# Optimization experiments

Measured on AMD Instinct MI355X. Metric: run time of the kernel, lower is better.

Reference implementation:

```python
import jax, jax.numpy as jnp
import numpy as np

N_NODES = 50000
N_EDGES = 1000000
N_GRAPHS = 256
ORIG = 92
ATOM = 64
NBR = 41
EPS = 1e-5


def _bn_train(h, gamma, beta):
    # BatchNorm1d in training mode: batch stats, biased variance
    mu = h.mean(axis=0)
    var = jnp.var(h, axis=0)
    return (h - mu) * jax.lax.rsqrt(var + EPS) * gamma + beta


def setup_inputs() -> dict:
    key = jax.random.key(0)
    ks = jax.random.split(key, 16)
    inp = {
        "x": jax.random.normal(ks[0], (N_NODES, ORIG), dtype=jnp.float32),
        "edge_attr": jax.random.normal(ks[1], (N_EDGES, NBR), dtype=jnp.float32),
        "lower_f": jax.random.normal(ks[2], (N_NODES, ATOM), dtype=jnp.float32),
        "edge_index": jax.random.randint(ks[3], (2, N_EDGES), 0, N_NODES, dtype=jnp.int32),
        "batch": jnp.sort(jax.random.randint(ks[4], (N_NODES,), 0, N_GRAPHS, dtype=jnp.int32)),
        # params
        "emb_W": jax.random.normal(ks[5], (ORIG, ATOM), dtype=jnp.float32) / np.sqrt(ORIG),
        "emb_b": jnp.zeros((ATOM,), dtype=jnp.float32),
        "fc_W": jax.random.normal(ks[6], (2 * ATOM + NBR, 2 * ATOM), dtype=jnp.float32) / np.sqrt(2 * ATOM + NBR),
        "fc_b": jnp.zeros((2 * ATOM,), dtype=jnp.float32),
        "bn1_g": jnp.ones((2 * ATOM,), dtype=jnp.float32),
        "bn1_b": jnp.zeros((2 * ATOM,), dtype=jnp.float32),
        "bn2_g": jnp.ones((ATOM,), dtype=jnp.float32),
        "bn2_b": jnp.zeros((ATOM,), dtype=jnp.float32),
        "att_W": jax.random.normal(ks[7], (ATOM, 1), dtype=jnp.float32) / np.sqrt(ATOM),
        "att_b": jnp.zeros((1,), dtype=jnp.float32),
        "out_W": jax.random.normal(ks[8], (ATOM, 1), dtype=jnp.float32) / np.sqrt(ATOM),
        "out_b": jnp.zeros((1,), dtype=jnp.float32),
    }
    return inp


def reference(x, edge_attr, lower_f, emb_W, emb_b, fc_W, fc_b, bn1_g, bn1_b,
              bn2_g, bn2_b, att_W, att_b, out_W, out_b, edge_index, batch):
    # embedding + lower-level features
    atom_fea = x @ emb_W + emb_b + lower_f  # [N, ATOM]

    # CGConv: gather endpoints, concat with edge features
    src, dst = edge_index[0], edge_index[1]
    total = jnp.concatenate([atom_fea[src], atom_fea[dst], edge_attr], axis=-1)  # [E, 2A+NBR]
    gated = _bn_train(total @ fc_W + fc_b, bn1_g, bn1_b)  # [E, 2A]
    nbr_filter, nbr_core = gated[:, :ATOM], gated[:, ATOM:]
    msg = jax.nn.sigmoid(nbr_filter) * jax.nn.softplus(nbr_core)  # [E, A]
    summed = jax.ops.segment_sum(msg, src, num_segments=N_NODES)  # [N, A]
    atom_out = _bn_train(summed, bn2_g, bn2_b)

    # SiLU + attentional aggregation per graph
    h = jax.nn.silu(atom_out)  # [N, A]
    logits = (h @ att_W + att_b)[:, 0]  # [N]
    seg_max = jax.ops.segment_max(logits, batch, num_segments=N_GRAPHS)
    e = jnp.exp(logits - seg_max[batch])
    denom = jax.ops.segment_sum(e, batch, num_segments=N_GRAPHS)
    alpha = e / denom[batch]  # [N]
    crys = jax.ops.segment_sum(alpha[:, None] * h, batch, num_segments=N_GRAPHS)  # [G, A]
    crys_fea = crys @ out_W + out_b  # [G, 1]
    return atom_out, crys_fea
```

## Files before the change

### kernel.cpp

```cpp
#include <hip/hip_runtime.h>
#include <math.h>

#define NN 50000
#define NE 1000000
#define NG 256
#define ORIGD 92
#define NBRD 41
#define NSPREAD 32
#define SCAN_B 256

typedef unsigned short u16;
typedef __attribute__((ext_vector_type(8))) short short8;
typedef __attribute__((ext_vector_type(4))) float f32x4;
typedef __attribute__((ext_vector_type(8))) float f32x8;

#define OFF_AFB     0
#define OFF_SUMMED  1600000
#define OFF_WT      4800000
#define OFF_BN1SPR  4812288
#define OFF_BN1SC   4820480
#define OFF_BN2ACC  4820736
#define OFF_BN2SC   4820864
#define OFF_ELOG    4820992
#define OFF_SEGMAX  4870992
#define OFF_DENOM   4871248
#define OFF_CNT     4871504
#define OFF_PTR     4921504
#define OFF_HEAD    4971504
#define OFF_BSUM    5021504
#define OFF_BOFS    5021760
#define OFF_EIDX    5022016
#define OFF_H       6022016
#define OFF_T2_END  70022016
#define OFF_P       70022016
#define OFF_T3_END  82822016
#define OFF_SRCC    82822016
#define OFF_DSTC    83822016
#define OFF_EAB     84822016
#define OFF_T4_END  108822016

__device__ __forceinline__ u16 f2b(float f) {
    unsigned u = __float_as_uint(f);
    return (u16)((u + 0x7FFFu + ((u >> 16) & 1u)) >> 16);
}
__device__ __forceinline__ float b2f(u16 u) {
    return __uint_as_float(((unsigned)u) << 16);
}
__device__ __forceinline__ float gate(float f, float cc) {
    float sig = __builtin_amdgcn_rcpf(1.f + __expf(-f));
    float sp  = fmaxf(cc, 0.f) + __logf(1.f + __expf(-fabsf(cc)));
    return sig * sp;
}
__device__ __forceinline__ float fsilu(float x) {
    return x * __builtin_amdgcn_rcpf(1.f + __expf(-x));
}

__global__ __launch_bounds__(256) void k_embed2(
    const float* __restrict__ x, const float* __restrict__ lf,
    const float* __restrict__ W, const float* __restrict__ b,
    u16* __restrict__ afb, const float* __restrict__ fcW,
    u16* __restrict__ wT3, u16* __restrict__ wP, float* __restrict__ ws)
{
    int gid = blockIdx.x * 256 + threadIdx.x;
    int n = gid >> 6, c = gid & 63;
    const float* xr = x + (long)n * ORIGD;
    float acc = b[c] + lf[gid];
#pragma unroll 4
    for (int k = 0; k < ORIGD; k++)
        acc = fmaf(xr[k], W[k * 64 + c], acc);
    afb[gid] = f2b(acc);

    if (blockIdx.x < 96) {
        int i = blockIdx.x * 256 + threadIdx.x;
        if (i < 8192) {
            int j = i >> 6, k = i & 63;
            wT3[i] = (k < NBRD) ? f2b(fcW[(128 + k) * 128 + j]) : (u16)0;
        } else {
            int i2 = i - 8192;
            int j = i2 >> 6, k = i2 & 63;
            int row = (j < 128) ? k : (64 + k);
            wP[i2] = f2b(fcW[row * 128 + (j & 127)]);
        }
    } else if (blockIdx.x < 336) {
        int zid = (blockIdx.x - 96) * 256 + threadIdx.x;
        if (zid < 8704) {
            ws[OFF_BN1SPR + zid] = 0.f;
        } else {
            int z2 = zid - 8704;
            if (z2 < 50512) ws[OFF_SEGMAX + z2] = 0.f;
        }
    }
}

__global__ void k_prepw(const float* __restrict__ fcW, u16* __restrict__ wT)
{
    int i = blockIdx.x * 256 + threadIdx.x;
    int j = i / 192, k = i - j * 192;
    wT[i] = (k < 169) ? f2b(fcW[k * 128 + j]) : (u16)0;
}

__global__ void k_prepw2(const float* __restrict__ fcW, u16* __restrict__ wT3,
                         u16* __restrict__ wP)
{
    int i = blockIdx.x * 256 + threadIdx.x;
    if (i < 8192) {
        int j = i >> 6, k = i & 63;
        wT3[i] = (k < NBRD) ? f2b(fcW[(128 + k) * 128 + j]) : (u16)0;
    } else {
        int i2 = i - 8192;
        int j = i2 >> 6, k = i2 & 63;
        int row = (j < 128) ? k : (64 + k);
        wP[i2] = f2b(fcW[row * 128 + (j & 127)]);
    }
}

__global__ __launch_bounds__(256) void k_embed(
    const float* __restrict__ x, const float* __restrict__ lf,
    const float* __restrict__ W, const float* __restrict__ b,
    u16* __restrict__ afb)
{
    int gid = blockIdx.x * 256 + threadIdx.x;
    int n = gid >> 6, c = gid & 63;
    const float* xr = x + (long)n * ORIGD;
    float acc = b[c] + lf[gid];
#pragma unroll 4
    for (int k = 0; k < ORIGD; k++)
        acc = fmaf(xr[k], W[k * 64 + c], acc);
    afb[gid] = f2b(acc);
}

template <int PACKED>
__global__ __launch_bounds__(256) void k_pnode(
    const u16* __restrict__ afb, const u16* __restrict__ wP, float* __restrict__ P)
{
    __shared__ __align__(16) u16 sB[64 * 72];
    const int tid = threadIdx.x;
    const int n0 = blockIdx.x * 64;

    for (int i = tid; i < 512; i += 256) {
        int r = i >> 3, c = i & 7;
        int n = n0 + r;
        short8 v = {0,0,0,0,0,0,0,0};
        if (n < NN) v = *(const short8*)(afb + (long)n * 64 + c * 8);
        *(short8*)(sB + r * 72 + c * 8) = v;
    }
    __syncthreads();

    const int lane = tid & 63, w = tid >> 6;
    const int n16 = lane & 15, quad = lane >> 4;
    short8 A[4][2];
#pragma unroll
    for (int m = 0; m < 4; m++) {
        const u16* base = wP + (16 * (w + 4 * m) + n16) * 64 + quad * 8;
        A[m][0] = *(const short8*)(base);
        A[m][1] = *(const short8*)(base + 32);
    }
    for (int t = 0; t < 4; t++) {
        const u16* row = sB + (16 * t + n16) * 72 + quad * 8;
        short8 b0 = *(const short8*)(row);
        short8 b1 = *(const short8*)(row + 32);
        int n = n0 + 16 * t + n16;
#pragma unroll
        for (int m = 0; m < 4; m++) {
            f32x4 acc = {0.f, 0.f, 0.f, 0.f};
            acc = __builtin_amdgcn_mfma_f32_16x16x32_bf16(A[m][0], b0, acc, 0, 0, 0);
            acc = __builtin_amdgcn_mfma_f32_16x16x32_bf16(A[m][1], b1, acc, 0, 0, 0);
            if (n < NN) {
                int M = w + 4 * m;
                int j;
                if (PACKED) {
                    int MM = M & 7;
                    j = ((M >> 3) * 128) + ((MM & 3) * 4 + quad) * 8 + ((MM >> 2) << 2);
                } else {
                    j = 16 * M + 4 * quad;
                }
                *(f32x4*)(P + (long)n * 256 + j) = acc;
            }
        }
    }
}

__global__ void k_hist(const int* __restrict__ ei, int* __restrict__ cnt)
{
    int e = blockIdx.x * 256 + threadIdx.x;
    if (e < NE) atomicAdd(&cnt[ei[e]], 1);
}

__global__ __launch_bounds__(1024) void k_scan1b(const int* __restrict__ cnt,
                                                 int* __restrict__ ptr,
                                                 int* __restrict__ head)
{
    __shared__ int sw[16];
    const int t = threadIdx.x;
    const int CH = (NN + 1023) / 1024;
    const int base = t * CH;
    int s = 0;
    for (int i = 0; i < CH; i++) {
        int n = base + i;
        s += (n < NN) ? cnt[n] : 0;
    }
    int lane = t & 63, wv = t >> 6;
    int v = s;
    for (int o = 1; o < 64; o <<= 1) {
        int x = __shfl_up(v, o, 64);
        if (lane >= o) v += x;
    }
    if (lane == 63) sw[wv] = v;
    __syncthreads();
    if (t == 0) {
        int acc = 0;
        for (int i = 0; i < 16; i++) { int x = sw[i]; sw[i] = acc; acc += x; }
    }
    __syncthreads();
    int p = sw[wv] + (v - s);
    for (int i = 0; i < CH; i++) {
        int n = base + i;
        if (n < NN) { ptr[n] = p; head[n] = p; p += cnt[n]; }
    }
}

__global__ void k_partial(const int* __restrict__ cnt, int* __restrict__ lofs,
                          int* __restrict__ bsum)
{
    __shared__ int sd[SCAN_B];
    int t = threadIdx.x, b = blockIdx.x, n = b * SCAN_B + t;
    int v = (n < NN) ? cnt[n] : 0;
    sd[t] = v; __syncthreads();
    for (int o = 1; o < SCAN_B; o <<= 1) {
        int x = (t >= o) ? sd[t - o] : 0;
        __syncthreads();
        sd[t] += x;
        __syncthreads();
    }
    if (n < NN) lofs[n] = sd[t] - v;
    if (t == SCAN_B - 1) bsum[b] = sd[t];
}

__global__ void k_scanb(const int* __restrict__ bsum, int* __restrict__ bofs, int nb)
{
    __shared__ int sd[256];
    int t = threadIdx.x;
    int v = (t < nb) ? bsum[t] : 0;
    sd[t] = v; __syncthreads();
    for (int o = 1; o < 256; o <<= 1) {
        int x = (t >= o) ? sd[t - o] : 0;
        __syncthreads();
        sd[t] += x;
        __syncthreads();
    }
    bofs[t] = sd[t] - v;
}

__global__ void k_addofs(int* __restrict__ ptr, const int* __restrict__ bofs,
                         int* __restrict__ head)
{
    int n = blockIdx.x * 256 + threadIdx.x;
    if (n < NN) {
        int p = ptr[n] + bofs[n >> 8];
        ptr[n] = p; head[n] = p;
    }
}

__global__ void k_fill(const int* __restrict__ ei, int* __restrict__ head,
                       int* __restrict__ eidx)
{
    int e = blockIdx.x * 256 + threadIdx.x;
    if (e < NE) {
        int pos = atomicAdd(&head[ei[e]], 1);
        eidx[pos] = e;
    }
}

__global__ __launch_bounds__(256) void k_fill3(
    const int* __restrict__ ei, const float* __restrict__ ea,
    int* __restrict__ head, int* __restrict__ srcC, int* __restrict__ dstC,
    u16* __restrict__ eaB)
{
    int e = blockIdx.x * 256 + threadIdx.x;
    if (e >= NE) return;
    int s = ei[e];
    int pos = atomicAdd(&head[s], 1);
    srcC[pos] = s;
    dstC[pos] = ei[NE + e];
    const float* row = ea + (long)e * NBRD;
    u16* orow = eaB + (long)pos * 48;
#pragma unroll
    for (int q = 0; q < 6; q++) {
        short8 v;
#pragma unroll
        for (int j = 0; j < 8; j++) {
            int c = q * 8 + j;
            v[j] = (c < NBRD) ? (short)f2b(row[c]) : (short)0;
        }
        *(short8*)(orow + q * 8) = v;
    }
}

__global__ __launch_bounds__(256) void k_gemm_h4(
    const u16* __restrict__ eaB, const int* __restrict__ srcC,
    const int* __restrict__ dstC, const u16* __restrict__ wT3,
    const float* __restrict__ P, u16* __restrict__ h,
    float* __restrict__ spread)
{
    const int tid = threadIdx.x;
    const int e0 = blockIdx.x * 64;
    const int lane = tid & 63, w = tid >> 6;
    const int n16 = lane & 15, quad = lane >> 4;

    short8 A0[2], A1[2];
    {
        const u16* a0 = wT3 + (16 * w + n16) * 64 + quad * 8;
        const u16* a1 = wT3 + (16 * (w + 4) + n16) * 64 + quad * 8;
        A0[0] = *(const short8*)(a0);  A0[1] = *(const short8*)(a0 + 32);
        A1[0] = *(const short8*)(a1);  A1[1] = *(const short8*)(a1 + 32);
    }

    const int j0 = 16 * w + 4 * quad;
    const int pofs = (w * 4 + quad) * 8;
    const short8 bz = {0,0,0,0,0,0,0,0};
    float s0[4] = {0,0,0,0}, q0[4] = {0,0,0,0}, s1[4] = {0,0,0,0}, q1[4] = {0,0,0,0};

#pragma unroll
    for (int t = 0; t < 4; t++) {
        const int pos = e0 + 16 * t + n16;
        const int src = srcC[pos];
        const int dst = dstC[pos];

        const u16* er = eaB + (long)pos * 48;
        short8 b0 = *(const short8*)(er + quad * 8);
        short8 b1 = bz;
        if (quad < 2) b1 = *(const short8*)(er + 32 + quad * 8);

        f32x8 gS = *(const f32x8*)(P + (long)src * 256 + pofs);
        f32x8 gD = *(const f32x8*)(P + (long)dst * 256 + 128 + pofs);

        f32x4 acc0 = {0.f, 0.f, 0.f, 0.f}, acc1 = {0.f, 0.f, 0.f, 0.f};
        acc0 = __builtin_amdgcn_mfma_f32_16x16x32_bf16(A0[0], b0, acc0, 0, 0, 0);
        acc0 = __builtin_amdgcn_mfma_f32_16x16x32_bf16(A0[1], b1, acc0, 0, 0, 0);
        acc1 = __builtin_amdgcn_mfma_f32_16x16x32_bf16(A1[0], b0, acc1, 0, 0, 0);
        acc1 = __builtin_amdgcn_mfma_f32_16x16x32_bf16(A1[1], b1, acc1, 0, 0, 0);

        u16 hv0[4], hv1[4];
#pragma unroll
        for (int r = 0; r < 4; r++) {
            float u0 = acc0[r] + gS[r] + gD[r];
            float u1 = acc1[r] + gS[4 + r] + gD[4 + r];
            s0[r] += u0; q0[r] = fmaf(u0, u0, q0[r]);
            s1[r] += u1; q1[r] = fmaf(u1, u1, q1[r]);
            hv0[r] = f2b(u0); hv1[r] = f2b(u1);
        }
        u16* hp = h + (long)pos * 128 + j0;
        ushort4 v0 = make_ushort4(hv0[0], hv0[1], hv0[2], hv0[3]);
        ushort4 v1 = make_ushort4(hv1[0], hv1[1], hv1[2], hv1[3]);
        *(ushort4*)hp = v0;
        *(ushort4*)(hp + 64) = v1;
    }

#pragma unroll
    for (int m = 1; m < 16; m <<= 1) {
#pragma unroll
        for (int r = 0; r < 4; r++) {
            s0[r] += __shfl_xor(s0[r], m); q0[r] += __shfl_xor(q0[r], m);
            s1[r] += __shfl_xor(s1[r], m); q1[r] += __shfl_xor(q1[r], m);
        }
    }
    if (n16 == 0) {
        float* sp = spread + (blockIdx.x & (NSPREAD - 1)) * 256;
#pragma unroll
        for (int r = 0; r < 4; r++) {
            atomicAdd(sp + j0 + r,       s0[r]);
            atomicAdd(sp + 128 + j0 + r, q0[r]);
            atomicAdd(sp + 64 + j0 + r,  s1[r]);
            atomicAdd(sp + 192 + j0 + r, q1[r]);
        }
    }
}

__global__ __launch_bounds__(256) void k_gemm_h2(
    const float* __restrict__ ea, const int* __restrict__ ei,
    const u16* __restrict__ wT3, const float* __restrict__ P,
    u16* __restrict__ h, float* __restrict__ spread)
{
    __shared__ __align__(16) u16 sTl[64 * 72];
    __shared__ int sSrc[64], sDst[64];
    const int tid = threadIdx.x;
    const int e0 = blockIdx.x * 64;

    if (tid < 64) sSrc[tid] = ei[e0 + tid];
    else if (tid < 128) sDst[tid - 64] = ei[NE + e0 + tid - 64];

    for (int i = tid; i < 64 * 64; i += 256) {
        int e = i >> 6, c = i & 63;
        float v = (c < NBRD) ? ea[(long)(e0 + e) * NBRD + c] : 0.f;
        sTl[e * 72 + c] = f2b(v);
    }
    __syncthreads();

    const int lane = tid & 63, w = tid >> 6;
    const int n16 = lane & 15, quad = lane >> 4;

    short8 A0[2], A1[2];
    {
        const u16* b0 = wT3 + (16 * w + n16) * 64 + quad * 8;
        const u16* b1 = wT3 + (16 * (w + 4) + n16) * 64 + quad * 8;
        A0[0] = *(const short8*)(b0);  A0[1] = *(const short8*)(b0 + 32);
        A1[0] = *(const short8*)(b1);  A1[1] = *(const short8*)(b1 + 32);
    }

    const int j0 = 16 * w + 4 * quad;
    float s0[4] = {0,0,0,0}, q0[4] = {0,0,0,0}, s1[4] = {0,0,0,0}, q1[4] = {0,0,0,0};

    for (int t = 0; t < 4; t++) {
        const int ge16 = 16 * t + n16;
        const int src = sSrc[ge16], dst = sDst[ge16];
        const float* pS = P + (long)src * 256;
        const float* pD = P + (long)dst * 256 + 128;
        f32x4 g0 = *(const f32x4*)(pS + j0);
        f32x4 g1 = *(const f32x4*)(pS + 64 + j0);
        f32x4 g2 = *(const f32x4*)(pD + j0);
        f32x4 g3 = *(const f32x4*)(pD + 64 + j0);

        const u16* row = sTl + ge16 * 72 + quad * 8;
        short8 b0 = *(const short8*)(row);
        short8 b1 = *(const short8*)(row + 32);
        f32x4 acc0 = {0.f, 0.f, 0.f, 0.f}, acc1 = {0.f, 0.f, 0.f, 0.f};
        acc0 = __builtin_amdgcn_mfma_f32_16x16x32_bf16(A0[0], b0, acc0, 0, 0, 0);
        acc0 = __builtin_amdgcn_mfma_f32_16x16x32_bf16(A0[1], b1, acc0, 0, 0, 0);
        acc1 = __builtin_amdgcn_mfma_f32_16x16x32_bf16(A1[0], b0, acc1, 0, 0, 0);
        acc1 = __builtin_amdgcn_mfma_f32_16x16x32_bf16(A1[1], b1, acc1, 0, 0, 0);

        u16 hv0[4], hv1[4];
#pragma unroll
        for (int r = 0; r < 4; r++) {
            float u0 = acc0[r] + g0[r] + g2[r];
            float u1 = acc1[r] + g1[r] + g3[r];
            s0[r] += u0; q0[r] = fmaf(u0, u0, q0[r]);
            s1[r] += u1; q1[r] = fmaf(u1, u1, q1[r]);
            hv0[r] = f2b(u0); hv1[r] = f2b(u1);
        }
        int ge = e0 + ge16;
        u16* hp = h + (long)ge * 128 + j0;
        ushort4 v0 = make_ushort4(hv0[0], hv0[1], hv0[2], hv0[3]);
        ushort4 v1 = make_ushort4(hv1[0], hv1[1], hv1[2], hv1[3]);
        *(ushort4*)hp = v0;
        *(ushort4*)(hp + 64) = v1;
    }

#pragma unroll
    for (int m = 1; m < 16; m <<= 1) {
#pragma unroll
        for (int r = 0; r < 4; r++) {
            s0[r] += __shfl_xor(s0[r], m); q0[r] += __shfl_xor(q0[r], m);
            s1[r] += __shfl_xor(s1[r], m); q1[r] += __shfl_xor(q1[r], m);
        }
    }
    if (n16 == 0) {
        float* sp = spread + (blockIdx.x & (NSPREAD - 1)) * 256;
#pragma unroll
        for (int r = 0; r < 4; r++) {
            atomicAdd(sp + j0 + r,       s0[r]);
            atomicAdd(sp + 128 + j0 + r, q0[r]);
            atomicAdd(sp + 64 + j0 + r,  s1[r]);
            atomicAdd(sp + 192 + j0 + r, q1[r]);
        }
    }
}

__global__ __launch_bounds__(256) void k_gemm_h(
    const u16* __restrict__ afb, const float* __restrict__ ea,
    const int* __restrict__ ei, const u16* __restrict__ wT,
    u16* __restrict__ h, float* __restrict__ spread)
{
    __shared__ __align__(16) u16 sTl[64 * 200];
    __shared__ int sSrc[64], sDst[64];
    const int tid = threadIdx.x;
    const int e0 = blockIdx.x * 64;

    if (tid < 64) sSrc[tid] = ei[e0 + tid];
    else if (tid < 128) sDst[tid - 64] = ei[NE + e0 + tid - 64];
    __syncthreads();

    for (int i = tid; i < 1024; i += 256) {
        int e = i >> 4, q = i & 15;
        const u16* g = (q < 8) ? (afb + (long)sSrc[e] * 64 + q * 8)
                               : (afb + (long)sDst[e] * 64 + (q - 8) * 8);
        *(short8*)(sTl + e * 200 + q * 8) = *(const short8*)g;
    }
    for (int i = tid; i < 64 * 64; i += 256) {
        int e = i >> 6, c = i & 63;
        float v = (c < NBRD) ? ea[(long)(e0 + e) * NBRD + c] : 0.f;
        sTl[e * 200 + 128 + c] = f2b(v);
    }
    __syncthreads();

    const int lane = tid & 63, w = tid >> 6;
    const int n16 = lane & 15, quad = lane >> 4;

    short8 A0[6], A1[6];
    {
        const u16* b0 = wT + (16 * w + n16) * 192 + quad * 8;
        const u16* b1 = wT + (16 * (w + 4) + n16) * 192 + quad * 8;
#pragma unroll
        for (int ks = 0; ks < 6; ks++) {
            A0[ks] = *(const short8*)(b0 + ks * 32);
            A1[ks] = *(const short8*)(b1 + ks * 32);
        }
    }

    const int j0 = 16 * w + 4 * quad;
    float s0[4] = {0,0,0,0}, q0[4] = {0,0,0,0}, s1[4] = {0,0,0,0}, q1[4] = {0,0,0,0};

    for (int t = 0; t < 4; t++) {
        const u16* row = sTl + (16 * t + n16) * 200 + quad * 8;
        f32x4 acc0 = {0.f, 0.f, 0.f, 0.f}, acc1 = {0.f, 0.f, 0.f, 0.f};
#pragma unroll
        for (int ks = 0; ks < 6; ks++) {
            short8 b = *(const short8*)(row + ks * 32);
            acc0 = __builtin_amdgcn_mfma_f32_16x16x32_bf16(A0[ks], b, acc0, 0, 0, 0);
            acc1 = __builtin_amdgcn_mfma_f32_16x16x32_bf16(A1[ks], b, acc1, 0, 0, 0);
        }
#pragma unroll
        for (int r = 0; r < 4; r++) {
            s0[r] += acc0[r]; q0[r] = fmaf(acc0[r], acc0[r], q0[r]);
            s1[r] += acc1[r]; q1[r] = fmaf(acc1[r], acc1[r], q1[r]);
        }
        int ge = e0 + 16 * t + n16;
        u16* hp = h + (long)ge * 128 + j0;
        ushort4 v0 = make_ushort4(f2b(acc0[0]), f2b(acc0[1]), f2b(acc0[2]), f2b(acc0[3]));
        ushort4 v1 = make_ushort4(f2b(acc1[0]), f2b(acc1[1]), f2b(acc1[2]), f2b(acc1[3]));
        *(ushort4*)hp = v0;
        *(ushort4*)(hp + 64) = v1;
    }

#pragma unroll
    for (int m = 1; m < 16; m <<= 1) {
#pragma unroll
        for (int r = 0; r < 4; r++) {
            s0[r] += __shfl_xor(s0[r], m); q0[r] += __shfl_xor(q0[r], m);
            s1[r] += __shfl_xor(s1[r], m); q1[r] += __shfl_xor(q1[r], m);
        }
    }
    if (n16 == 0) {
        float* sp = spread + (blockIdx.x & (NSPREAD - 1)) * 256;
#pragma unroll
        for (int r = 0; r < 4; r++) {
            atomicAdd(sp + j0 + r,       s0[r]);
            atomicAdd(sp + 128 + j0 + r, q0[r]);
            atomicAdd(sp + 64 + j0 + r,  s1[r]);
            atomicAdd(sp + 192 + j0 + r, q1[r]);
        }
    }
}

template <int MODE>
__global__ __launch_bounds__(256) void k_gemm(
    const u16* __restrict__ afb, const float* __restrict__ ea,
    const int* __restrict__ ei, const u16* __restrict__ wT,
    const float* __restrict__ sc, float* __restrict__ outbuf)
{
    __shared__ __align__(16) u16 sTl[64 * 200];
    __shared__ int sSrc[64], sDst[64];
    const int tid = threadIdx.x;
    const int e0 = blockIdx.x * 64;

    if (tid < 64) sSrc[tid] = ei[e0 + tid];
    else if (tid < 128) sDst[tid - 64] = ei[NE + e0 + tid - 64];
    __syncthreads();
    for (int i = tid; i < 1024; i += 256) {
        int e = i >> 4, q = i & 15;
        const u16* g = (q < 8) ? (afb + (long)sSrc[e] * 64 + q * 8)
                               : (afb + (long)sDst[e] * 64 + (q - 8) * 8);
        *(short8*)(sTl + e * 200 + q * 8) = *(const short8*)g;
    }
    for (int i = tid; i < 64 * 64; i += 256) {
        int e = i >> 6, c = i & 63;
        float v = (c < NBRD) ? ea[(long)(e0 + e) * NBRD + c] : 0.f;
        sTl[e * 200 + 128 + c] = f2b(v);
    }
    __syncthreads();

    const int lane = tid & 63, w = tid >> 6;
    const int n16 = lane & 15, quad = lane >> 4;
    short8 A0[6], A1[6];
    {
        const u16* b0 = wT + (16 * w + n16) * 192 + quad * 8;
        const u16* b1 = wT + (16 * (w + 4) + n16) * 192 + quad * 8;
#pragma unroll
        for (int ks = 0; ks < 6; ks++) {
            A0[ks] = *(const short8*)(b0 + ks * 32);
            A1[ks] = *(const short8*)(b1 + ks * 32);
        }
    }
    const int j0 = 16 * w + 4 * quad;
    float s0[4] = {0,0,0,0}, q0[4] = {0,0,0,0}, s1[4] = {0,0,0,0}, q1[4] = {0,0,0,0};
    float scf[4], shf[4], scc[4], shc[4];
    if (MODE == 1) {
#pragma unroll
        for (int r = 0; r < 4; r++) {
            scf[r] = sc[j0 + r];        shf[r] = sc[128 + j0 + r];
            scc[r] = sc[64 + j0 + r];   shc[r] = sc[192 + j0 + r];
        }
    }
    for (int t = 0; t < 4; t++) {
        const u16* row = sTl + (16 * t + n16) * 200 + quad * 8;
        f32x4 acc0 = {0.f, 0.f, 0.f, 0.f}, acc1 = {0.f, 0.f, 0.f, 0.f};
#pragma unroll
        for (int ks = 0; ks < 6; ks++) {
            short8 b = *(const short8*)(row + ks * 32);
            acc0 = __builtin_amdgcn_mfma_f32_16x16x32_bf16(A0[ks], b, acc0, 0, 0, 0);
            acc1 = __builtin_amdgcn_mfma_f32_16x16x32_bf16(A1[ks], b, acc1, 0, 0, 0);
        }
        if (MODE == 0) {
#pragma unroll
            for (int r = 0; r < 4; r++) {
                s0[r] += acc0[r]; q0[r] = fmaf(acc0[r], acc0[r], q0[r]);
                s1[r] += acc1[r]; q1[r] = fmaf(acc1[r], acc1[r], q1[r]);
            }
        } else {
            int src = sSrc[16 * t + n16];
            float* dst = outbuf + (long)src * 64 + j0;
#pragma unroll
            for (int r = 0; r < 4; r++) {
                float f  = fmaf(acc0[r], scf[r], shf[r]);
                float cc = fmaf(acc1[r], scc[r], shc[r]);
                atomicAdd(dst + r, gate(f, cc));
            }
        }
    }
    if (MODE == 0) {
#pragma unroll
        for (int m = 1; m < 16; m <<= 1) {
#pragma unroll
            for (int r = 0; r < 4; r++) {
                s0[r] += __shfl_xor(s0[r], m); q0[r] += __shfl_xor(q0[r], m);
                s1[r] += __shfl_xor(s1[r], m); q1[r] += __shfl_xor(q1[r], m);
            }
        }
        if (n16 == 0) {
            float* sp = outbuf + (blockIdx.x & (NSPREAD - 1)) * 256;
#pragma unroll
            for (int r = 0; r < 4; r++) {
                atomicAdd(sp + j0 + r,       s0[r]);
                atomicAdd(sp + 128 + j0 + r, q0[r]);
                atomicAdd(sp + 64 + j0 + r,  s1[r]);
                atomicAdd(sp + 192 + j0 + r, q1[r]);
            }
        }
    }
}

__global__ void k_bn1fin(const float* __restrict__ spread,
                         const float* __restrict__ g, const float* __restrict__ b,
                         float* __restrict__ sc)
{
    int c = threadIdx.x;
    float s = 0.f, q = 0.f;
    for (int k = 0; k < NSPREAD; k++) { s += spread[k * 256 + c]; q += spread[k * 256 + 128 + c]; }
    float mean_acc = s / (float)NE;
    float var = q / (float)NE - mean_acc * mean_acc;
    float scale = g[c] * rsqrtf(var + 1e-5f);
    sc[c] = scale;
    sc[128 + c] = b[c] - mean_acc * scale;
}

__global__ __launch_bounds__(256) void k_scatter3(
    const u16* __restrict__ h, const int* __restrict__ ptr,
    const int* __restrict__ cnt, const float* __restrict__ spread,
    const float* __restrict__ g, const float* __restrict__ b,
    float* __restrict__ summed)
{
    __shared__ float ssc[256];
    int tid = threadIdx.x;
    if (tid < 128) {
        int c = tid;
        float s = 0.f, q = 0.f;
        for (int k = 0; k < NSPREAD; k++) {
            s += spread[k * 256 + c]; q += spread[k * 256 + 128 + c];
        }
        float mean_acc = s / (float)NE;
        float var = q / (float)NE - mean_acc * mean_acc;
        float scale = g[c] * rsqrtf(var + 1e-5f);
        ssc[c] = scale;
        ssc[128 + c] = b[c] - mean_acc * scale;
    }
    __syncthreads();

    int n = blockIdx.x * 4 + (tid >> 6);
    int l = tid & 63;
    int es = l & 7, cg = l >> 3;

    float scf[8], shf[8], scc[8], shc[8];
#pragma unroll
    for (int j = 0; j < 8; j++) {
        scf[j] = ssc[cg * 8 + j];
        shf[j] = ssc[128 + cg * 8 + j];
        scc[j] = ssc[64 + cg * 8 + j];
        shc[j] = ssc[192 + cg * 8 + j];
    }

    int p0 = ptr[n], deg = cnt[n];
    float acc[8] = {0,0,0,0,0,0,0,0};
    for (int i = 0; i < deg; i += 8) {
        int idx = i + es;
        bool valid = idx < deg;
        int row = p0 + (valid ? idx : 0);
        const u16* hr = h + (long)row * 128;
        short8 f8 = *(const short8*)(hr + cg * 8);
        short8 c8 = *(const short8*)(hr + 64 + cg * 8);
#pragma unroll
        for (int j = 0; j < 8; j++) {
            float f  = fmaf(b2f((u16)f8[j]), scf[j], shf[j]);
            float cc = fmaf(b2f((u16)c8[j]), scc[j], shc[j]);
            float gg = gate(f, cc);
            acc[j] += valid ? gg : 0.f;
        }
    }
#pragma unroll
    for (int m = 1; m < 8; m <<= 1)
#pragma unroll
        for (int j = 0; j < 8; j++) acc[j] += __shfl_xor(acc[j], m);
    if (es == 0) {
        float* sp = summed + (long)n * 64 + cg * 8;
        float4 v0 = {acc[0], acc[1], acc[2], acc[3]};
        float4 v1 = {acc[4], acc[5], acc[6], acc[7]};
        *(float4*)sp = v0;
        *(float4*)(sp + 4) = v1;
    }
}

__global__ __launch_bounds__(256) void k_scatter(
    const u16* __restrict__ h, const int* __restrict__ ptr,
    const int* __restrict__ cnt, const int* __restrict__ eidx,
    const float* __restrict__ sc, float* __restrict__ summed)
{
    int tid = threadIdx.x;
    int n = blockIdx.x * 4 + (tid >> 6);
    int l = tid & 63;
    int es = l & 7, cg = l >> 3;

    float4 a0 = *(const float4*)(sc + cg * 8);
    float4 a1 = *(const float4*)(sc + cg * 8 + 4);
    float4 b0 = *(const float4*)(sc + 128 + cg * 8);
    float4 b1 = *(const float4*)(sc + 128 + cg * 8 + 4);
    float4 c0 = *(const float4*)(sc + 64 + cg * 8);
    float4 c1 = *(const float4*)(sc + 64 + cg * 8 + 4);
    float4 d0 = *(const float4*)(sc + 192 + cg * 8);
    float4 d1 = *(const float4*)(sc + 192 + cg * 8 + 4);
    float scf[8] = {a0.x,a0.y,a0.z,a0.w,a1.x,a1.y,a1.z,a1.w};
    float shf[8] = {b0.x,b0.y,b0.z,b0.w,b1.x,b1.y,b1.z,b1.w};
    float scc[8] = {c0.x,c0.y,c0.z,c0.w,c1.x,c1.y,c1.z,c1.w};
    float shc[8] = {d0.x,d0.y,d0.z,d0.w,d1.x,d1.y,d1.z,d1.w};

    int p0 = ptr[n], deg = cnt[n];
    float acc[8] = {0,0,0,0,0,0,0,0};
    for (int i = 0; i < deg; i += 8) {
        int idx = i + es;
        bool valid = idx < deg;
        int e = eidx[p0 + (valid ? idx : 0)];
        const u16* hr = h + (long)e * 128;
        short8 f8 = *(const short8*)(hr + cg * 8);
        short8 c8 = *(const short8*)(hr + 64 + cg * 8);
#pragma unroll
        for (int j = 0; j < 8; j++) {
            float f  = fmaf(b2f((u16)f8[j]), scf[j], shf[j]);
            float cc = fmaf(b2f((u16)c8[j]), scc[j], shc[j]);
            float gg = gate(f, cc);
            acc[j] += valid ? gg : 0.f;
        }
    }
#pragma unroll
    for (int m = 1; m < 8; m <<= 1)
#pragma unroll
        for (int j = 0; j < 8; j++) acc[j] += __shfl_xor(acc[j], m);
    if (es == 0) {
        float* sp = summed + (long)n * 64 + cg * 8;
        float4 v0 = {acc[0], acc[1], acc[2], acc[3]};
        float4 v1 = {acc[4], acc[5], acc[6], acc[7]};
        *(float4*)sp = v0;
        *(float4*)(sp + 4) = v1;
    }
}

__global__ __launch_bounds__(256) void k_bn2stats(const float* __restrict__ summed,
                                                  float* __restrict__ acc2)
{
    int tid = threadIdx.x; int c = tid & 63; int sub = tid >> 6;
    float s = 0.f, q = 0.f;
    for (int r = blockIdx.x * 4 + sub; r < NN; r += 4 * 128) {
        float v = summed[(long)r * 64 + c]; s += v; q = fmaf(v, v, q);
    }
    __shared__ float rs[256], rq[256];
    rs[tid] = s; rq[tid] = q; __syncthreads();
    if (tid < 64) {
        s = rs[tid] + rs[tid + 64] + rs[tid + 128] + rs[tid + 192];
        q = rq[tid] + rq[tid + 64] + rq[tid + 128] + rq[tid + 192];
        atomicAdd(&acc2[tid], s);
        atomicAdd(&acc2[64 + tid], q);
    }
}

__global__ void k_bn2fin(const float* __restrict__ acc2,
                         const float* __restrict__ g, const float* __restrict__ b,
                         float* __restrict__ sc2, const float* __restrict__ outb,
                         float* __restrict__ out)
{
    int c = threadIdx.x;
    if (c < 64) {
        float mean = acc2[c] / (float)NN;
        float var = acc2[64 + c] / (float)NN - mean * mean;
        float scale = g[c] * rsqrtf(var + 1e-5f);
        sc2[c] = scale;
        sc2[64 + c] = b[c] - mean * scale;
    }
    out[(long)NN * 64 + c] = outb[0];
}

__global__ __launch_bounds__(256) void k_nodepost2(
    const float* __restrict__ summed, const float* __restrict__ acc2,
    const float* __restrict__ g, const float* __restrict__ b,
    const float* __restrict__ attW, const float* __restrict__ attb,
    const int* __restrict__ batch, float* __restrict__ out,
    float* __restrict__ elog, unsigned* __restrict__ segmax)
{
    __shared__ float ssc2[128];
    int tid = threadIdx.x;
    if (tid < 64) {
        float mean = acc2[tid] / (float)NN;
        float var = acc2[64 + tid] / (float)NN - mean * mean;
        float scale = g[tid] * rsqrtf(var + 1e-5f);
        ssc2[tid] = scale;
        ssc2[64 + tid] = b[tid] - mean * scale;
    }
    __syncthreads();

    int n = blockIdx.x * 4 + (tid >> 6); int c = tid & 63;
    float v = summed[(long)n * 64 + c];
    float ao = fmaf(v, ssc2[c], ssc2[64 + c]);
    out[(long)n * 64 + c] = ao;
    float h = fsilu(ao);
    float p = h * attW[c];
#pragma unroll
    for (int off = 32; off; off >>= 1) p += __shfl_down(p, off, 64);
    if (c == 0) {
        float logit = p + attb[0];
        elog[n] = logit;
        unsigned u = __float_as_uint(logit);
        u = (u & 0x80000000u) ? ~u : (u | 0x80000000u);
        atomicMax(&segmax[batch[n]], u);
    }
}

__global__ __launch_bounds__(256) void k_nodepost(
    const float* __restrict__ summed, const float* __restrict__ sc2,
    const float* __restrict__ attW, const float* __restrict__ attb,
    const int* __restrict__ batch, float* __restrict__ out,
    float* __restrict__ elog, unsigned* __restrict__ segmax)
{
    int tid = threadIdx.x; int n = blockIdx.x * 4 + (tid >> 6); int c = tid & 63;
    float v = summed[(long)n * 64 + c];
    float ao = fmaf(v, sc2[c], sc2[64 + c]);
    out[(long)n * 64 + c] = ao;
    float h = fsilu(ao);
    float p = h * attW[c];
#pragma unroll
    for (int off = 32; off; off >>= 1) p += __shfl_down(p, off, 64);
    if (c == 0) {
        float logit = p + attb[0];
        elog[n] = logit;
        unsigned u = __float_as_uint(logit);
        u = (u & 0x80000000u) ? ~u : (u | 0x80000000u);
        atomicMax(&segmax[batch[n]], u);
    }
}

__global__ void k_denom2(const int* __restrict__ batch,
                         const unsigned* __restrict__ segmax,
                         float* __restrict__ elog, float* __restrict__ denom,
                         const float* __restrict__ outb, float* __restrict__ out)
{
    int n = blockIdx.x * 256 + threadIdx.x;
    if (n < NG) out[(long)NN * 64 + n] = outb[0];
    if (n >= NN) return;
    int b = batch[n];
    unsigned u = segmax[b];
    u = (u & 0x80000000u) ? (u & 0x7FFFFFFFu) : ~u;
    float e = __expf(elog[n] - __uint_as_float(u));
    elog[n] = e;
    atomicAdd(&denom[b], e);
}

__global__ void k_denom(const int* __restrict__ batch,
                        const unsigned* __restrict__ segmax,
                        float* __restrict__ elog, float* __restrict__ denom)
{
    int n = blockIdx.x * 256 + threadIdx.x;
    if (n >= NN) return;
    int b = batch[n];
    unsigned u = segmax[b];
    u = (u & 0x80000000u) ? (u & 0x7FFFFFFFu) : ~u;
    float e = __expf(elog[n] - __uint_as_float(u));
    elog[n] = e;
    atomicAdd(&denom[b], e);
}

__global__ __launch_bounds__(256) void k_crys(
    const float* __restrict__ atom_out, const float* __restrict__ elog,
    const float* __restrict__ denom, const int* __restrict__ batch,
    const float* __restrict__ outW, float* __restrict__ out)
{
    int tid = threadIdx.x; int n = blockIdx.x * 4 + (tid >> 6); int l = tid & 63;
    int b = batch[n];
    float alpha = elog[n] / denom[b];
    float ao = atom_out[(long)n * 64 + l];
    float p = fsilu(ao) * outW[l];
#pragma unroll
    for (int off = 32; off; off >>= 1) p += __shfl_down(p, off, 64);
    if (l == 0) atomicAdd(&out[(long)NN * 64 + b], alpha * p);
}

extern "C" void kernel_launch(void* const* d_in, const int* in_sizes, int n_in,
                              void* d_out, int out_size, void* d_ws, size_t ws_size,
                              hipStream_t stream)
{
    const float* x    = (const float*)d_in[0];
    const float* eatt = (const float*)d_in[1];
    const float* lf   = (const float*)d_in[2];
    const int*   ei   = (const int*)d_in[3];
    const int*   batch= (const int*)d_in[4];
    const float* embW = (const float*)d_in[5];
    const float* embB = (const float*)d_in[6];
    const float* fcW  = (const float*)d_in[7];
    const float* bn1g = (const float*)d_in[9];
    const float* bn1b = (const float*)d_in[10];
    const float* bn2g = (const float*)d_in[11];
    const float* bn2b = (const float*)d_in[12];
    const float* attW = (const float*)d_in[13];
    const float* attB = (const float*)d_in[14];
    const float* outW = (const float*)d_in[15];
    const float* outB = (const float*)d_in[16];
    float* out = (float*)d_out;
    float* ws  = (float*)d_ws;

    u16* afb  = (u16*)(ws + OFF_AFB);
    u16* wT   = (u16*)(ws + OFF_WT);
    int* cnt  = (int*)(ws + OFF_CNT);
    int* ptr  = (int*)(ws + OFF_PTR);
    int* head = (int*)(ws + OFF_HEAD);
    int* bsum = (int*)(ws + OFF_BSUM);
    int* bofs = (int*)(ws + OFF_BOFS);
    int* eidx = (int*)(ws + OFF_EIDX);
    u16* h    = (u16*)(ws + OFF_H);

    const bool t4 = ws_size >= (size_t)OFF_T4_END * sizeof(float);
    const bool t3 = ws_size >= (size_t)OFF_T3_END * sizeof(float);
    const bool t2 = ws_size >= (size_t)OFF_T2_END * sizeof(float);

    if (t4) {
        u16* wT3  = wT;
        u16* wP   = wT + 8192;
        float* P  = ws + OFF_P;
        int* srcC = (int*)(ws + OFF_SRCC);
        int* dstC = (int*)(ws + OFF_DSTC);
        u16* eaB  = (u16*)(ws + OFF_EAB);
        k_embed2<<<12500, 256, 0, stream>>>(x, lf, embW, embB, afb, fcW, wT3, wP, ws);
        k_hist<<<(NE + 255) / 256, 256, 0, stream>>>(ei, cnt);
        k_scan1b<<<1, 1024, 0, stream>>>(cnt, ptr, head);
        k_fill3<<<(NE + 255) / 256, 256, 0, stream>>>(ei, eatt, head, srcC, dstC, eaB);
        k_pnode<1><<<(NN + 63) / 64, 256, 0, stream>>>(afb, wP, P);
        k_gemm_h4<<<NE / 64, 256, 0, stream>>>(eaB, srcC, dstC, wT3, P, h,
                                               ws + OFF_BN1SPR);
        k_scatter3<<<NN / 4, 256, 0, stream>>>(h, ptr, cnt, ws + OFF_BN1SPR,
                                               bn1g, bn1b, ws + OFF_SUMMED);
        k_bn2stats<<<128, 256, 0, stream>>>(ws + OFF_SUMMED, ws + OFF_BN2ACC);
        k_nodepost2<<<12500, 256, 0, stream>>>(ws + OFF_SUMMED, ws + OFF_BN2ACC,
                                               bn2g, bn2b, attW, attB, batch, out,
                                               ws + OFF_ELOG,
                                               (unsigned*)(ws + OFF_SEGMAX));
        k_denom2<<<196, 256, 0, stream>>>(batch, (const unsigned*)(ws + OFF_SEGMAX),
                                          ws + OFF_ELOG, ws + OFF_DENOM, outB, out);
        k_crys<<<12500, 256, 0, stream>>>(out, ws + OFF_ELOG, ws + OFF_DENOM, batch,
                                          outW, out);
        return;
    }

    k_embed<<<12500, 256, 0, stream>>>(x, lf, embW, embB, afb);

    if (t3) {
        u16* wT3 = wT;
        u16* wP  = wT + 8192;
        float* P = ws + OFF_P;
        k_prepw2<<<96, 256, 0, stream>>>(fcW, wT3, wP);
        hipMemsetAsync(ws + OFF_BN1SPR, 0,
                       (size_t)(OFF_PTR - OFF_BN1SPR) * sizeof(float), stream);
        k_hist<<<(NE + 255) / 256, 256, 0, stream>>>(ei, cnt);
        k_partial<<<(NN + SCAN_B - 1) / SCAN_B, SCAN_B, 0, stream>>>(cnt, ptr, bsum);
        k_scanb<<<1, 256, 0, stream>>>(bsum, bofs, (NN + SCAN_B - 1) / SCAN_B);
        k_addofs<<<(NN + 255) / 256, 256, 0, stream>>>(ptr, bofs, head);
        k_fill<<<(NE + 255) / 256, 256, 0, stream>>>(ei, head, eidx);
        k_pnode<0><<<(NN + 63) / 64, 256, 0, stream>>>(afb, wP, P);
        k_gemm_h2<<<NE / 64, 256, 0, stream>>>(eatt, ei, wT3, P, h, ws + OFF_BN1SPR);
        k_bn1fin<<<1, 128, 0, stream>>>(ws + OFF_BN1SPR, bn1g, bn1b, ws + OFF_BN1SC);
        k_scatter<<<NN / 4, 256, 0, stream>>>(h, ptr, cnt, eidx, ws + OFF_BN1SC,
                                              ws + OFF_SUMMED);
    } else if (t2) {
        k_prepw<<<96, 256, 0, stream>>>(fcW, wT);
        hipMemsetAsync(ws + OFF_BN1SPR, 0,
                       (size_t)(OFF_PTR - OFF_BN1SPR) * sizeof(float), stream);
        k_hist<<<(NE + 255) / 256, 256, 0, stream>>>(ei, cnt);
        k_partial<<<(NN + SCAN_B - 1) / SCAN_B, SCAN_B, 0, stream>>>(cnt, ptr, bsum);
        k_scanb<<<1, 256, 0, stream>>>(bsum, bofs, (NN + SCAN_B - 1) / SCAN_B);
        k_addofs<<<(NN + 255) / 256, 256, 0, stream>>>(ptr, bofs, head);
        k_fill<<<(NE + 255) / 256, 256, 0, stream>>>(ei, head, eidx);
        k_gemm_h<<<NE / 64, 256, 0, stream>>>(afb, eatt, ei, wT, h, ws + OFF_BN1SPR);
        k_bn1fin<<<1, 128, 0, stream>>>(ws + OFF_BN1SPR, bn1g, bn1b, ws + OFF_BN1SC);
        k_scatter<<<NN / 4, 256, 0, stream>>>(h, ptr, cnt, eidx, ws + OFF_BN1SC,
                                              ws + OFF_SUMMED);
    } else {
        k_prepw<<<96, 256, 0, stream>>>(fcW, wT);
        hipMemsetAsync(ws + OFF_SUMMED, 0,
                       (size_t)(OFF_PTR - OFF_SUMMED) * sizeof(float), stream);
        k_gemm<0><<<NE / 64, 256, 0, stream>>>(afb, eatt, ei, wT, ws + OFF_BN1SC,
                                               ws + OFF_BN1SPR);
        k_bn1fin<<<1, 128, 0, stream>>>(ws + OFF_BN1SPR, bn1g, bn1b, ws + OFF_BN1SC);
        k_gemm<1><<<NE / 64, 256, 0, stream>>>(afb, eatt, ei, wT, ws + OFF_BN1SC,
                                               ws + OFF_SUMMED);
    }

    k_bn2stats<<<128, 256, 0, stream>>>(ws + OFF_SUMMED, ws + OFF_BN2ACC);
    k_bn2fin<<<1, 256, 0, stream>>>(ws + OFF_BN2ACC, bn2g, bn2b, ws + OFF_BN2SC,
                                    outB, out);
    k_nodepost<<<12500, 256, 0, stream>>>(ws + OFF_SUMMED, ws + OFF_BN2SC, attW, attB,
                                          batch, out, ws + OFF_ELOG,
                                          (unsigned*)(ws + OFF_SEGMAX));
    k_denom<<<196, 256, 0, stream>>>(batch, (const unsigned*)(ws + OFF_SEGMAX),
                                     ws + OFF_ELOG, ws + OFF_DENOM);
    k_crys<<<12500, 256, 0, stream>>>(out, ws + OFF_ELOG, ws + OFF_DENOM, batch,
                                      outW, out);
}
```

Baseline: 1.280 ms.

## Convert edge_attr in original order, use multi-block scan, prefetch edge loads in GEMM

Edge-attribute bf16 conversion moves out of the atomic fill into the histogram kernel, which converts each edge row coalesced in original order with six threads per edge. The fill kernel now writes only the permutation and the src/dst arrays, and the GEMM gathers edge rows through the permutation index. The single-block 1024-thread scan is replaced by the existing three-kernel multi-block scan. The GEMM software-pipelines its gathers with double buffering and sets occupancy launch bounds, trading a random read of edge rows in the GEMM for coalesced conversion writes.

After: 1.194 ms. 6.7% less time.

```diff
diff --git a/kernel.cpp b/kernel.cpp
--- a/kernel.cpp
+++ b/kernel.cpp
@@ -186,37 +186,24 @@
     if (e < NE) atomicAdd(&cnt[ei[e]], 1);
 }
 
-__global__ __launch_bounds__(1024) void k_scan1b(const int* __restrict__ cnt,
-                                                 int* __restrict__ ptr,
-                                                 int* __restrict__ head)
-{
-    __shared__ int sw[16];
-    const int t = threadIdx.x;
-    const int CH = (NN + 1023) / 1024;
-    const int base = t * CH;
-    int s = 0;
-    for (int i = 0; i < CH; i++) {
-        int n = base + i;
-        s += (n < NN) ? cnt[n] : 0;
-    }
-    int lane = t & 63, wv = t >> 6;
-    int v = s;
-    for (int o = 1; o < 64; o <<= 1) {
-        int x = __shfl_up(v, o, 64);
-        if (lane >= o) v += x;
-    }
-    if (lane == 63) sw[wv] = v;
-    __syncthreads();
-    if (t == 0) {
-        int acc = 0;
-        for (int i = 0; i < 16; i++) { int x = sw[i]; sw[i] = acc; acc += x; }
-    }
-    __syncthreads();
-    int p = sw[wv] + (v - s);
-    for (int i = 0; i < CH; i++) {
-        int n = base + i;
-        if (n < NN) { ptr[n] = p; head[n] = p; p += cnt[n]; }
-    }
+__global__ __launch_bounds__(256) void k_hist2(
+    const int* __restrict__ ei, const float* __restrict__ ea,
+    int* __restrict__ cnt, u16* __restrict__ eaB)
+{
+    long gid = (long)blockIdx.x * 256 + threadIdx.x;
+    if (gid >= (long)NE * 6) return;
+    int e = (int)(gid / 6);
+    int q = (int)(gid - (long)e * 6);
+    if (q == 0) atomicAdd(&cnt[ei[e]], 1);
+    const float* row = ea + (long)e * NBRD;
+    int c0 = q * 8;
+    short8 v;
+#pragma unroll
+    for (int j = 0; j < 8; j++) {
+        int c = c0 + j;
+        v[j] = (c < NBRD) ? (short)f2b(row[c]) : (short)0;
+    }
+    *(short8*)(eaB + (long)e * 48 + c0) = v;
 }
 
 __global__ void k_partial(const int* __restrict__ cnt, int* __restrict__ lofs,
@@ -271,36 +258,25 @@
     }
 }
 
-__global__ __launch_bounds__(256) void k_fill3(
-    const int* __restrict__ ei, const float* __restrict__ ea,
-    int* __restrict__ head, int* __restrict__ srcC, int* __restrict__ dstC,
-    u16* __restrict__ eaB)
+__global__ void k_fill2(const int* __restrict__ ei, int* __restrict__ head,
+                        int* __restrict__ eidx, int* __restrict__ srcC,
+                        int* __restrict__ dstC)
 {
     int e = blockIdx.x * 256 + threadIdx.x;
-    if (e >= NE) return;
-    int s = ei[e];
-    int pos = atomicAdd(&head[s], 1);
-    srcC[pos] = s;
-    dstC[pos] = ei[NE + e];
-    const float* row = ea + (long)e * NBRD;
-    u16* orow = eaB + (long)pos * 48;
-#pragma unroll
-    for (int q = 0; q < 6; q++) {
-        short8 v;
-#pragma unroll
-        for (int j = 0; j < 8; j++) {
-            int c = q * 8 + j;
-            v[j] = (c < NBRD) ? (short)f2b(row[c]) : (short)0;
-        }
-        *(short8*)(orow + q * 8) = v;
-    }
-}
-
-__global__ __launch_bounds__(256) void k_gemm_h4(
-    const u16* __restrict__ eaB, const int* __restrict__ srcC,
-    const int* __restrict__ dstC, const u16* __restrict__ wT3,
-    const float* __restrict__ P, u16* __restrict__ h,
-    float* __restrict__ spread)
+    if (e < NE) {
+        int s = ei[e];
+        int pos = atomicAdd(&head[s], 1);
+        eidx[pos] = e;
+        srcC[pos] = s;
+        dstC[pos] = ei[NE + e];
+    }
+}
+
+__global__ __launch_bounds__(256, 4) void k_gemm_h5(
+    const u16* __restrict__ eaB, const int* __restrict__ eidx,
+    const int* __restrict__ srcC, const int* __restrict__ dstC,
+    const u16* __restrict__ wT3, const float* __restrict__ P,
+    u16* __restrict__ h, float* __restrict__ spread)
 {
     const int tid = threadIdx.x;
     const int e0 = blockIdx.x * 64;
@@ -320,41 +296,54 @@
     const short8 bz = {0,0,0,0,0,0,0,0};
     float s0[4] = {0,0,0,0}, q0[4] = {0,0,0,0}, s1[4] = {0,0,0,0}, q1[4] = {0,0,0,0};
 
-#pragma unroll
-    for (int t = 0; t < 4; t++) {
-        const int pos = e0 + 16 * t + n16;
-        const int src = srcC[pos];
-        const int dst = dstC[pos];
-
-        const u16* er = eaB + (long)pos * 48;
-        short8 b0 = *(const short8*)(er + quad * 8);
-        short8 b1 = bz;
-        if (quad < 2) b1 = *(const short8*)(er + 32 + quad * 8);
-
-        f32x8 gS = *(const f32x8*)(P + (long)src * 256 + pofs);
-        f32x8 gD = *(const f32x8*)(P + (long)dst * 256 + 128 + pofs);
-
-        f32x4 acc0 = {0.f, 0.f, 0.f, 0.f}, acc1 = {0.f, 0.f, 0.f, 0.f};
-        acc0 = __builtin_amdgcn_mfma_f32_16x16x32_bf16(A0[0], b0, acc0, 0, 0, 0);
-        acc0 = __builtin_amdgcn_mfma_f32_16x16x32_bf16(A0[1], b1, acc0, 0, 0, 0);
-        acc1 = __builtin_amdgcn_mfma_f32_16x16x32_bf16(A1[0], b0, acc1, 0, 0, 0);
-        acc1 = __builtin_amdgcn_mfma_f32_16x16x32_bf16(A1[1], b1, acc1, 0, 0, 0);
-
-        u16 hv0[4], hv1[4];
-#pragma unroll
-        for (int r = 0; r < 4; r++) {
-            float u0 = acc0[r] + gS[r] + gD[r];
-            float u1 = acc1[r] + gS[4 + r] + gD[4 + r];
-            s0[r] += u0; q0[r] = fmaf(u0, u0, q0[r]);
-            s1[r] += u1; q1[r] = fmaf(u1, u1, q1[r]);
-            hv0[r] = f2b(u0); hv1[r] = f2b(u1);
-        }
-        u16* hp = h + (long)pos * 128 + j0;
-        ushort4 v0 = make_ushort4(hv0[0], hv0[1], hv0[2], hv0[3]);
-        ushort4 v1 = make_ushort4(hv1[0], hv1[1], hv1[2], hv1[3]);
-        *(ushort4*)hp = v0;
-        *(ushort4*)(hp + 64) = v1;
-    }
+    short8 b0A, b1A, b0B, b1B;
+    f32x8 gSA, gDA, gSB, gDB;
+
+#define LOADT(t, b0v, b1v, gSv, gDv)                                       \
+    {                                                                      \
+        int p_ = e0 + 16 * (t) + n16;                                      \
+        int s_ = srcC[p_], d_ = dstC[p_], e_ = eidx[p_];                   \
+        const u16* er_ = eaB + (long)e_ * 48;                              \
+        b0v = *(const short8*)(er_ + quad * 8);                            \
+        b1v = (quad < 2) ? *(const short8*)(er_ + 32 + quad * 8) : bz;     \
+        gSv = *(const f32x8*)(P + (long)s_ * 256 + pofs);                  \
+        gDv = *(const f32x8*)(P + (long)d_ * 256 + 128 + pofs);            \
+    }
+
+#define COMPT(t, b0v, b1v, gSv, gDv)                                       \
+    {                                                                      \
+        f32x4 acc0 = {0.f,0.f,0.f,0.f}, acc1 = {0.f,0.f,0.f,0.f};          \
+        acc0 = __builtin_amdgcn_mfma_f32_16x16x32_bf16(A0[0], b0v, acc0, 0, 0, 0); \
+        acc0 = __builtin_amdgcn_mfma_f32_16x16x32_bf16(A0[1], b1v, acc0, 0, 0, 0); \
+        acc1 = __builtin_amdgcn_mfma_f32_16x16x32_bf16(A1[0], b0v, acc1, 0, 0, 0); \
+        acc1 = __builtin_amdgcn_mfma_f32_16x16x32_bf16(A1[1], b1v, acc1, 0, 0, 0); \
+        u16 hv0[4], hv1[4];                                                \
+        _Pragma("unroll")                                                  \
+        for (int r = 0; r < 4; r++) {                                      \
+            float u0 = acc0[r] + gSv[r] + gDv[r];                          \
+            float u1 = acc1[r] + gSv[4 + r] + gDv[4 + r];                  \
+            s0[r] += u0; q0[r] = fmaf(u0, u0, q0[r]);                      \
+            s1[r] += u1; q1[r] = fmaf(u1, u1, q1[r]);                      \
+            hv0[r] = f2b(u0); hv1[r] = f2b(u1);                            \
+        }                                                                  \
+        u16* hp = h + (long)(e0 + 16 * (t) + n16) * 128 + j0;              \
+        ushort4 v0 = make_ushort4(hv0[0], hv0[1], hv0[2], hv0[3]);         \
+        ushort4 v1 = make_ushort4(hv1[0], hv1[1], hv1[2], hv1[3]);         \
+        *(ushort4*)hp = v0;                                                \
+        *(ushort4*)(hp + 64) = v1;                                         \
+    }
+
+    LOADT(0, b0A, b1A, gSA, gDA);
+    LOADT(1, b0B, b1B, gSB, gDB);
+    COMPT(0, b0A, b1A, gSA, gDA);
+    LOADT(2, b0A, b1A, gSA, gDA);
+    COMPT(1, b0B, b1B, gSB, gDB);
+    LOADT(3, b0B, b1B, gSB, gDB);
+    COMPT(2, b0A, b1A, gSA, gDA);
+    COMPT(3, b0B, b1B, gSB, gDB);
+
+#undef LOADT
+#undef COMPT
 
 #pragma unroll
     for (int m = 1; m < 16; m <<= 1) {
@@ -963,11 +952,13 @@
         int* dstC = (int*)(ws + OFF_DSTC);
         u16* eaB  = (u16*)(ws + OFF_EAB);
         k_embed2<<<12500, 256, 0, stream>>>(x, lf, embW, embB, afb, fcW, wT3, wP, ws);
-        k_hist<<<(NE + 255) / 256, 256, 0, stream>>>(ei, cnt);
-        k_scan1b<<<1, 1024, 0, stream>>>(cnt, ptr, head);
-        k_fill3<<<(NE + 255) / 256, 256, 0, stream>>>(ei, eatt, head, srcC, dstC, eaB);
+        k_hist2<<<(NE * 6 + 255) / 256, 256, 0, stream>>>(ei, eatt, cnt, eaB);
+        k_partial<<<(NN + SCAN_B - 1) / SCAN_B, SCAN_B, 0, stream>>>(cnt, ptr, bsum);
+        k_scanb<<<1, 256, 0, stream>>>(bsum, bofs, (NN + SCAN_B - 1) / SCAN_B);
+        k_addofs<<<(NN + 255) / 256, 256, 0, stream>>>(ptr, bofs, head);
+        k_fill2<<<(NE + 255) / 256, 256, 0, stream>>>(ei, head, eidx, srcC, dstC);
         k_pnode<1><<<(NN + 63) / 64, 256, 0, stream>>>(afb, wP, P);
-        k_gemm_h4<<<NE / 64, 256, 0, stream>>>(eaB, srcC, dstC, wT3, P, h,
+        k_gemm_h5<<<NE / 64, 256, 0, stream>>>(eaB, eidx, srcC, dstC, wT3, P, h,
                                                ws + OFF_BN1SPR);
         k_scatter3<<<NN / 4, 256, 0, stream>>>(h, ptr, cnt, ws + OFF_BN1SPR,
                                                bn1g, bn1b, ws + OFF_SUMMED);
```
